# Optimization experiments

Measured on AMD Instinct MI355X. Metric: run time of the kernel, lower is better.

## Reference

```python
import jax, jax.numpy as jnp
import numpy as np

D_MODEL = 1024
NUM_HEADS = 16
D_K = D_MODEL // NUM_HEADS
B, S = 4, 2048


def setup_inputs() -> dict:
    key = jax.random.key(0)
    ks = jax.random.split(key, 12)
    scale = 1.0 / np.sqrt(D_MODEL)
    inp = {
        "Q": jax.random.normal(ks[0], (B, S, D_MODEL), dtype=jnp.float32),
        "K": jax.random.normal(ks[1], (B, S, D_MODEL), dtype=jnp.float32),
        "V": jax.random.normal(ks[2], (B, S, D_MODEL), dtype=jnp.float32),
        # causal mask broadcast over batch and heads; masked_fill where mask==0
        "mask": jnp.tril(jnp.ones((S, S), dtype=jnp.int32))[None, None, :, :],
        "Wq": jax.random.normal(ks[3], (D_MODEL, D_MODEL), dtype=jnp.float32) * scale,
        "bq": jnp.zeros((D_MODEL,), dtype=jnp.float32),
        "Wk": jax.random.normal(ks[4], (D_MODEL, D_MODEL), dtype=jnp.float32) * scale,
        "bk": jnp.zeros((D_MODEL,), dtype=jnp.float32),
        "Wv": jax.random.normal(ks[5], (D_MODEL, D_MODEL), dtype=jnp.float32) * scale,
        "bv": jnp.zeros((D_MODEL,), dtype=jnp.float32),
        "Wo": jax.random.normal(ks[6], (D_MODEL, D_MODEL), dtype=jnp.float32) * scale,
        "bo": jnp.zeros((D_MODEL,), dtype=jnp.float32),
    }
    return inp


def _split_heads(x):
    b, s, _ = x.shape
    return x.reshape(b, s, NUM_HEADS, D_K).transpose(0, 2, 1, 3)  # [B,H,S,Dk]


def reference(Q, K, V, mask, Wq, bq, Wk, bk, Wv, bv, Wo, bo):
    # torch nn.Linear: x @ W.T + b
    q = _split_heads(Q @ Wq.T + bq)
    k = _split_heads(K @ Wk.T + bk)
    v = _split_heads(V @ Wv.T + bv)
    scores = jnp.einsum("bhsd,bhtd->bhst", q, k) / jnp.sqrt(jnp.float32(D_K))
    scores = jnp.where(mask == 0, jnp.float32(-1e9), scores)
    probs = jax.nn.softmax(scores, axis=-1)  # dropout is identity in eval mode
    ctx = jnp.einsum("bhst,bhtd->bhsd", probs, v)
    ctx = ctx.transpose(0, 2, 1, 3).reshape(Q.shape[0], Q.shape[1], D_MODEL)
    out = ctx @ Wo.T + bo
    return out, probs
```

## Files before the change

kernel.cpp:

```cpp
#include <hip/hip_runtime.h>
#include <stdint.h>

typedef unsigned short u16;
typedef unsigned int u32;
typedef __attribute__((ext_vector_type(2))) unsigned int u32x2;
typedef __attribute__((ext_vector_type(8))) short short8;
typedef __attribute__((ext_vector_type(4))) float f32x4;
typedef __attribute__((ext_vector_type(4))) unsigned int u32x4;

#define SEQ 2048
#define DM 1024
#define NH 16
#define NBH 64
#define MR 8192

#define GLOAD16(g, l) __builtin_amdgcn_global_load_lds( \
    (const __attribute__((address_space(1))) void*)(g), \
    (__attribute__((address_space(3))) void*)(l), 16, 0, 0)

#define VMCNT(N) asm volatile("s_waitcnt vmcnt(" #N ")" ::: "memory")

__device__ __forceinline__ u16 f2bf(float f) {
  u32 u = __float_as_uint(f);
  u32 r = u + 0x7fffu + ((u >> 16) & 1u);
  return (u16)(r >> 16);
}
__device__ __forceinline__ u32 cvtpk_bf16(float lo, float hi) {
  u32 r;
  asm("v_cvt_pk_bf16_f32 %0, %1, %2" : "=v"(r) : "v"(lo), "v"(hi));
  return r;
}

__global__ __launch_bounds__(256) void cvt_all(
    const float* __restrict__ Q, const float* __restrict__ K, const float* __restrict__ V,
    const float* __restrict__ Wq, const float* __restrict__ Wk, const float* __restrict__ Wv,
    const float* __restrict__ Wo,
    u16* __restrict__ dQ, u16* __restrict__ dK, u16* __restrict__ dV,
    u16* __restrict__ dWq, u16* __restrict__ dWk, u16* __restrict__ dWv, u16* __restrict__ dWo) {
  int b = blockIdx.x;
  const float* s; u16* d; size_t off;
  if (b < 4096)       { s = Q;  d = dQ;  off = (size_t)b * 2048; }
  else if (b < 8192)  { s = K;  d = dK;  off = (size_t)(b - 4096) * 2048; }
  else if (b < 12288) { s = V;  d = dV;  off = (size_t)(b - 8192) * 2048; }
  else if (b < 12800) { s = Wq; d = dWq; off = (size_t)(b - 12288) * 2048; }
  else if (b < 13312) { s = Wk; d = dWk; off = (size_t)(b - 12800) * 2048; }
  else if (b < 13824) { s = Wv; d = dWv; off = (size_t)(b - 13312) * 2048; }
  else                { s = Wo; d = dWo; off = (size_t)(b - 13824) * 2048; }
  size_t i = off + (size_t)threadIdx.x * 8;
  float4 x = *(const float4*)(s + i);
  float4 y = *(const float4*)(s + i + 4);
  u32x4 o;
  o.x = (u32)f2bf(x.x) | ((u32)f2bf(x.y) << 16);
  o.y = (u32)f2bf(x.z) | ((u32)f2bf(x.w) << 16);
  o.z = (u32)f2bf(y.x) | ((u32)f2bf(y.y) << 16);
  o.w = (u32)f2bf(y.z) | ((u32)f2bf(y.w) << 16);
  *(u32x4*)(d + i) = o;
}

template <int MODE>
__global__ __launch_bounds__(256) void gemm_bt(
    const u16* __restrict__ A, const u16* __restrict__ Bw, const float* __restrict__ bias,
    void* __restrict__ Cp) {
  const int bid = blockIdx.x;
  const int wg = (bid & 7) * 64 + (bid >> 3);
  const int bn = wg & 7;
  const int bm = wg >> 3;
  __shared__ u16 As[128 * 64];
  __shared__ u16 Bs[128 * 64];
  const int tid = threadIdx.x;
  const int lane = tid & 63, wave = tid >> 6;
  const int wr = wave >> 1, wc = wave & 1;
  const int g16 = lane >> 4, l16 = lane & 15;
  f32x4 acc[4][4] = {};

  const int srow = lane >> 3;
  const int scol = (lane & 7) * 8;
  const u16* Abase = A + (size_t)(bm * 128) * DM + scol;
  const u16* Bbase = Bw + (size_t)(bn * 128) * DM + scol;

  for (int kt = 0; kt < DM; kt += 64) {
    __syncthreads();
#pragma unroll
    for (int i = 0; i < 4; ++i) {
      const int r0 = wave * 32 + i * 8;
      GLOAD16(Abase + (size_t)(r0 + srow) * DM + kt, (char*)As + r0 * 128);
      GLOAD16(Bbase + (size_t)(r0 + srow) * DM + kt, (char*)Bs + r0 * 128);
    }
    __syncthreads();
#pragma unroll
    for (int ks = 0; ks < 2; ++ks) {
      short8 af[4], bfr[4];
#pragma unroll
      for (int m = 0; m < 4; ++m)
        af[m] = *(const short8*)((const char*)As + (wr * 64 + m * 16 + l16) * 128 + ks * 64 + g16 * 16);
#pragma unroll
      for (int n = 0; n < 4; ++n)
        bfr[n] = *(const short8*)((const char*)Bs + (wc * 64 + n * 16 + l16) * 128 + ks * 64 + g16 * 16);
#pragma unroll
      for (int m = 0; m < 4; ++m)
#pragma unroll
        for (int n = 0; n < 4; ++n)
          acc[m][n] = __builtin_amdgcn_mfma_f32_16x16x32_bf16(af[m], bfr[n], acc[m][n], 0, 0, 0);
    }
  }
#pragma unroll
  for (int m = 0; m < 4; ++m)
#pragma unroll
    for (int n = 0; n < 4; ++n) {
      int col = bn * 128 + wc * 64 + n * 16 + l16;
      float bs = bias[col];
      if (MODE == 2) {
        int row0 = bm * 128 + wr * 64 + m * 16 + g16 * 4;
        int bb = row0 >> 11, ss = row0 & 2047;
        int hh = col >> 6, dd = col & 63;
        u32 lo = (u32)f2bf(acc[m][n][0] + bs) | ((u32)f2bf(acc[m][n][1] + bs) << 16);
        u32 hi = (u32)f2bf(acc[m][n][2] + bs) | ((u32)f2bf(acc[m][n][3] + bs) << 16);
        *(u32x2*)((u16*)Cp + (((size_t)(bb * NH + hh) * 64 + dd) * SEQ + ss)) = (u32x2){lo, hi};
      } else {
#pragma unroll
        for (int r = 0; r < 4; ++r) {
          int row = bm * 128 + wr * 64 + m * 16 + g16 * 4 + r;
          float v = acc[m][n][r] + bs;
          if (MODE == 0) {
            int bb = row >> 11, ss = row & 2047, hh = col >> 6, dd = col & 63;
            ((u16*)Cp)[((((size_t)bb * NH + hh) * SEQ + ss) << 6) + dd] = f2bf(v);
          } else {
            ((float*)Cp)[(size_t)row * DM + col] = v;
          }
        }
      }
    }
}

__global__ __launch_bounds__(512, 4) void attn_fwd(
    const u16* __restrict__ qh, const u16* __restrict__ kh, const u16* __restrict__ vt,
    float* __restrict__ probs, u16* __restrict__ ctx) {
  const int bid = blockIdx.x;
  const int wg = (bid & 7) * 128 + (bid >> 3);
  const int qt = 15 - (wg & 15);
  const int bh = wg >> 4;
  const int tid = threadIdx.x;
  const int lane = tid & 63, wave = tid >> 6;
  const int g16 = lane >> 4, l16 = lane & 15;
  __shared__ __align__(16) char SLDS[65536];
  char* Ps = SLDS + 49152;

  const int qglob = qt * 128 + wave * 16 + l16;
  short8 qf0, qf1;
  {
    const u16* qp = qh + ((size_t)bh * SEQ + qglob) * 64 + g16 * 8;
    qf0 = *(const short8*)qp;
    qf1 = *(const short8*)(qp + 32);
  }
  float lrow = 0.f;
  const float SL2 = 0.125f * 1.44269504088896f;

  const int srow = wave * 8 + (lane >> 3);
  const int sblk = (lane & 7) ^ (lane >> 3);
  const u16* kS = kh + ((size_t)bh * SEQ + srow) * 64 + sblk * 8;
  const u16* vS = vt + ((size_t)bh * 64 + srow) * SEQ + sblk * 8;

  auto qk64 = [&](const char* Kb, int ss, f32x4 (&sc)[4]) {
#pragma unroll
    for (int ks = 0; ks < 2; ++ks) {
      const short8 qf = ks ? qf1 : qf0;
#pragma unroll
      for (int f = 0; f < 4; ++f) {
        const int t = ss * 64 + f * 16 + l16;
        const short8 kb = *(const short8*)(Kb + ((t * 128 + ks * 64 + g16 * 16) ^ ((t & 7) << 4)));
        sc[f] = __builtin_amdgcn_mfma_f32_16x16x32_bf16(kb, qf, sc[f], 0, 0, 0);
      }
    }
  };

  const int nkA = qt + 1;
  auto stageA = [&](int kt) {
#pragma unroll
    for (int i = 0; i < 2; ++i)
      GLOAD16(kS + ((size_t)kt * 128 + i * 64) * 64,
              SLDS + (kt % 3) * 16384 + i * 8192 + wave * 1024);
  };
  stageA(0);
  for (int kt = 0; kt < nkA; ++kt) {
    if (kt + 1 < nkA) { stageA(kt + 1); VMCNT(2); }
    else VMCNT(0);
    __builtin_amdgcn_s_barrier();
    const char* Kb = SLDS + (kt % 3) * 16384;
    float s = 0.f;
#pragma unroll
    for (int ss = 0; ss < 2; ++ss) {
      f32x4 sc[4] = {};
      __builtin_amdgcn_s_setprio(1);
      qk64(Kb, ss, sc);
      __builtin_amdgcn_s_setprio(0);
#pragma unroll
      for (int f = 0; f < 4; ++f)
#pragma unroll
        for (int r = 0; r < 4; ++r) {
          const int k = kt * 128 + ss * 64 + f * 16 + g16 * 4 + r;
          s += (k <= qglob) ? exp2f(sc[f][r] * SL2) : 0.f;
        }
    }
    s += __shfl_xor(s, 16);
    s += __shfl_xor(s, 32);
    lrow += s;
  }
  const float rinv = 1.f / lrow;

  f32x4 acc[4] = {};
  const size_t prowB = ((size_t)bh * SEQ + qglob) * SEQ;
  const int prow = wave * 16 + l16;
  const int nkt = 2 * qt + 2;

  __syncthreads();
  auto stageBK = [&](int kt) {
    GLOAD16(kS + (size_t)kt * 4096, SLDS + (kt % 3) * 8192 + wave * 1024);
  };
  auto stageBV = [&](int kt) {
    GLOAD16(vS + (size_t)kt * 64, SLDS + 24576 + (kt % 3) * 8192 + wave * 1024);
  };
  stageBK(0); stageBV(0);
  for (int kt = 0; kt < nkt; ++kt) {
    if (kt + 1 < nkt) {
      stageBK(kt + 1); stageBV(kt + 1);
      if (kt == 0) VMCNT(2); else VMCNT(6);
    } else {
      if (kt == 0) VMCNT(0); else VMCNT(4);
    }
    __builtin_amdgcn_s_barrier();
    const char* Kb = SLDS + (kt % 3) * 8192;
    const char* Vb = SLDS + 24576 + (kt % 3) * 8192;
    f32x4 sc[4] = {};
    __builtin_amdgcn_s_setprio(1);
    qk64(Kb, 0, sc);
    __builtin_amdgcn_s_setprio(0);
#pragma unroll
    for (int f = 0; f < 4; ++f) {
      float pv[4];
#pragma unroll
      for (int r = 0; r < 4; ++r) {
        const int k = kt * 64 + f * 16 + g16 * 4 + r;
        pv[r] = (k <= qglob) ? exp2f(sc[f][r] * SL2) * rinv : 0.f;
      }
      *(float4*)(probs + prowB + kt * 64 + f * 16 + g16 * 4) =
          (float4){pv[0], pv[1], pv[2], pv[3]};
      u32x2 pk = {cvtpk_bf16(pv[0], pv[1]), cvtpk_bf16(pv[2], pv[3])};
      *(u32x2*)(Ps + ((prow * 128 + f * 32 + g16 * 8) ^ ((prow & 7) << 4))) = pk;
    }
    __builtin_amdgcn_s_setprio(1);
#pragma unroll
    for (int ks = 0; ks < 2; ++ks) {
      const short8 pa = *(const short8*)(Ps + ((prow * 128 + ks * 64 + g16 * 16) ^ ((prow & 7) << 4)));
#pragma unroll
      for (int cf = 0; cf < 4; ++cf) {
        const int dd = cf * 16 + l16;
        const short8 vb = *(const short8*)(Vb + ((dd * 128 + ks * 64 + g16 * 16) ^ ((dd & 7) << 4)));
        acc[cf] = __builtin_amdgcn_mfma_f32_16x16x32_bf16(pa, vb, acc[cf], 0, 0, 0);
      }
    }
    __builtin_amdgcn_s_setprio(0);
  }

  {
    const size_t zrow = ((size_t)bh * SEQ + qt * 128 + wave * 16 + (lane >> 2)) * SEQ;
    const int pcol = (lane & 3) * 16;
    const float4 z = {0.f, 0.f, 0.f, 0.f};
    for (int c0 = nkt * 64 + pcol; c0 < SEQ; c0 += 64) {
      float* dst = probs + zrow + c0;
      *(float4*)(dst) = z;
      *(float4*)(dst + 4) = z;
      *(float4*)(dst + 8) = z;
      *(float4*)(dst + 12) = z;
    }
  }

#pragma unroll
  for (int cf = 0; cf < 4; ++cf)
#pragma unroll
    for (int r = 0; r < 4; ++r) {
      const int srw = qt * 128 + wave * 16 + g16 * 4 + r;
      const size_t o = ((size_t)(bh >> 4) * SEQ + srw) * DM + (bh & 15) * 64 + cf * 16 + l16;
      ctx[o] = f2bf(acc[cf][r]);
    }
}

extern "C" void kernel_launch(void* const* d_in, const int* in_sizes, int n_in,
                              void* d_out, int out_size, void* d_ws, size_t ws_size,
                              hipStream_t stream) {
  (void)in_sizes; (void)n_in; (void)out_size; (void)ws_size;
  const float* Q  = (const float*)d_in[0];
  const float* K  = (const float*)d_in[1];
  const float* V  = (const float*)d_in[2];
  const float* Wq = (const float*)d_in[4];
  const float* bq = (const float*)d_in[5];
  const float* Wk = (const float*)d_in[6];
  const float* bk = (const float*)d_in[7];
  const float* Wv = (const float*)d_in[8];
  const float* bv = (const float*)d_in[9];
  const float* Wo = (const float*)d_in[10];
  const float* bo = (const float*)d_in[11];

  char* ws = (char*)d_ws;
  const size_t MB = 1024 * 1024;
  u16* Qb  = (u16*)(ws + 0 * MB);
  u16* Kb  = (u16*)(ws + 16 * MB);
  u16* Vb  = (u16*)(ws + 32 * MB);
  u16* Wqb = (u16*)(ws + 48 * MB);
  u16* Wkb = (u16*)(ws + 50 * MB);
  u16* Wvb = (u16*)(ws + 52 * MB);
  u16* Wob = (u16*)(ws + 54 * MB);
  u16* qhp = (u16*)(ws + 56 * MB);
  u16* khp = (u16*)(ws + 72 * MB);
  u16* vtp = (u16*)(ws + 88 * MB);
  u16* ctx = Kb;

  float* outp = (float*)d_out;
  float* probs = outp + (size_t)MR * DM;

  cvt_all<<<14336, 256, 0, stream>>>(Q, K, V, Wq, Wk, Wv, Wo, Qb, Kb, Vb, Wqb, Wkb, Wvb, Wob);
  gemm_bt<0><<<512, 256, 0, stream>>>(Qb, Wqb, bq, qhp);
  gemm_bt<0><<<512, 256, 0, stream>>>(Kb, Wkb, bk, khp);
  gemm_bt<2><<<512, 256, 0, stream>>>(Vb, Wvb, bv, vtp);
  attn_fwd<<<1024, 512, 0, stream>>>(qhp, khp, vtp, probs, ctx);
  gemm_bt<1><<<512, 256, 0, stream>>>(ctx, Wob, bo, outp);
}
```

Measured before the change: 505.0 us.

## Fuse QKV GEMMs, deepen K prefetch, use nontemporal stores for outputs

The three Q/K/V projection GEMMs become one 1536-block launch that picks its operands by block index, removing two kernel launches and letting the three GEMMs run concurrently. The attention row-sum pass now prefetches K two tiles ahead over four LDS buffers instead of one tile ahead over three. The large probs writes, including the zero-fill of masked regions, and the final fp32 output now use nontemporal stores to reduce cache pollution from the write stream. The fourth K buffer overlaps the Ps region of LDS, which is safe only if pass A never touches Ps.

```diff
diff --git a/kernel.cpp b/kernel.cpp
--- a/kernel.cpp
+++ b/kernel.cpp
@@ -57,12 +57,9 @@
   *(u32x4*)(d + i) = o;
 }
 
-template <int MODE>
-__global__ __launch_bounds__(256) void gemm_bt(
+__device__ __forceinline__ void gemm_body(
     const u16* __restrict__ A, const u16* __restrict__ Bw, const float* __restrict__ bias,
-    void* __restrict__ Cp) {
-  const int bid = blockIdx.x;
-  const int wg = (bid & 7) * 64 + (bid >> 3);
+    void* __restrict__ Cp, int wg, int MODE) {
   const int bn = wg & 7;
   const int bm = wg >> 3;
   __shared__ u16 As[128 * 64];
@@ -125,11 +122,32 @@
             int bb = row >> 11, ss = row & 2047, hh = col >> 6, dd = col & 63;
             ((u16*)Cp)[((((size_t)bb * NH + hh) * SEQ + ss) << 6) + dd] = f2bf(v);
           } else {
-            ((float*)Cp)[(size_t)row * DM + col] = v;
+            __builtin_nontemporal_store(v, (float*)Cp + (size_t)row * DM + col);
           }
         }
       }
     }
+}
+
+__global__ __launch_bounds__(256) void gemm_qkv(
+    const u16* __restrict__ Qb, const u16* __restrict__ Wqb, const float* __restrict__ bq, u16* __restrict__ qhp,
+    const u16* __restrict__ Kb, const u16* __restrict__ Wkb, const float* __restrict__ bk, u16* __restrict__ khp,
+    const u16* __restrict__ Vb, const u16* __restrict__ Wvb, const float* __restrict__ bv, u16* __restrict__ vtp) {
+  const int bid = blockIdx.x;
+  const int sel = bid >> 9;
+  const int inner = bid & 511;
+  const int wg = (inner & 7) * 64 + (inner >> 3);
+  if (sel == 0)      gemm_body(Qb, Wqb, bq, qhp, wg, 0);
+  else if (sel == 1) gemm_body(Kb, Wkb, bk, khp, wg, 0);
+  else               gemm_body(Vb, Wvb, bv, vtp, wg, 2);
+}
+
+__global__ __launch_bounds__(256) void gemm_out(
+    const u16* __restrict__ A, const u16* __restrict__ Bw, const float* __restrict__ bias,
+    float* __restrict__ Cp) {
+  const int bid = blockIdx.x;
+  const int wg = (bid & 7) * 64 + (bid >> 3);
+  gemm_body(A, Bw, bias, Cp, wg, 1);
 }
 
 __global__ __launch_bounds__(512, 4) void attn_fwd(
@@ -178,14 +196,16 @@
 #pragma unroll
     for (int i = 0; i < 2; ++i)
       GLOAD16(kS + ((size_t)kt * 128 + i * 64) * 64,
-              SLDS + (kt % 3) * 16384 + i * 8192 + wave * 1024);
+              SLDS + (kt & 3) * 16384 + i * 8192 + wave * 1024);
   };
   stageA(0);
+  if (nkA > 1) stageA(1);
   for (int kt = 0; kt < nkA; ++kt) {
-    if (kt + 1 < nkA) { stageA(kt + 1); VMCNT(2); }
+    if (kt + 2 < nkA) { stageA(kt + 2); VMCNT(4); }
+    else if (kt + 1 < nkA) VMCNT(2);
     else VMCNT(0);
     __builtin_amdgcn_s_barrier();
-    const char* Kb = SLDS + (kt % 3) * 16384;
+    const char* Kb = SLDS + (kt & 3) * 16384;
     float s = 0.f;
 #pragma unroll
     for (int ss = 0; ss < 2; ++ss) {
@@ -242,8 +262,8 @@
         const int k = kt * 64 + f * 16 + g16 * 4 + r;
         pv[r] = (k <= qglob) ? exp2f(sc[f][r] * SL2) * rinv : 0.f;
       }
-      *(float4*)(probs + prowB + kt * 64 + f * 16 + g16 * 4) =
-          (float4){pv[0], pv[1], pv[2], pv[3]};
+      __builtin_nontemporal_store((f32x4){pv[0], pv[1], pv[2], pv[3]},
+                                  (f32x4*)(probs + prowB + kt * 64 + f * 16 + g16 * 4));
       u32x2 pk = {cvtpk_bf16(pv[0], pv[1]), cvtpk_bf16(pv[2], pv[3])};
       *(u32x2*)(Ps + ((prow * 128 + f * 32 + g16 * 8) ^ ((prow & 7) << 4))) = pk;
     }
@@ -264,13 +284,13 @@
   {
     const size_t zrow = ((size_t)bh * SEQ + qt * 128 + wave * 16 + (lane >> 2)) * SEQ;
     const int pcol = (lane & 3) * 16;
-    const float4 z = {0.f, 0.f, 0.f, 0.f};
+    const f32x4 z = {0.f, 0.f, 0.f, 0.f};
     for (int c0 = nkt * 64 + pcol; c0 < SEQ; c0 += 64) {
       float* dst = probs + zrow + c0;
-      *(float4*)(dst) = z;
-      *(float4*)(dst + 4) = z;
-      *(float4*)(dst + 8) = z;
-      *(float4*)(dst + 12) = z;
+      __builtin_nontemporal_store(z, (f32x4*)(dst));
+      __builtin_nontemporal_store(z, (f32x4*)(dst + 4));
+      __builtin_nontemporal_store(z, (f32x4*)(dst + 8));
+      __builtin_nontemporal_store(z, (f32x4*)(dst + 12));
     }
   }
 
@@ -318,9 +338,7 @@
   float* probs = outp + (size_t)MR * DM;
 
   cvt_all<<<14336, 256, 0, stream>>>(Q, K, V, Wq, Wk, Wv, Wo, Qb, Kb, Vb, Wqb, Wkb, Wvb, Wob);
-  gemm_bt<0><<<512, 256, 0, stream>>>(Qb, Wqb, bq, qhp);
-  gemm_bt<0><<<512, 256, 0, stream>>>(Kb, Wkb, bk, khp);
-  gemm_bt<2><<<512, 256, 0, stream>>>(Vb, Wvb, bv, vtp);
+  gemm_qkv<<<1536, 256, 0, stream>>>(Qb, Wqb, bq, qhp, Kb, Wkb, bk, khp, Vb, Wvb, bv, vtp);
   attn_fwd<<<1024, 512, 0, stream>>>(qhp, khp, vtp, probs, ctx);
-  gemm_bt<1><<<512, 256, 0, stream>>>(ctx, Wob, bo, outp);
-}
+  gemm_out<<<512, 256, 0, stream>>>(ctx, Wob, bo, outp);
+}
```

New measurement: 1.075 ms. 2.13x slower.
